# Performance work log

Measured on AMD Instinct MI355X. Metric: run time of the kernel, lower is better.

Reference implementation:

```python
import jax, jax.numpy as jnp
import numpy as np

B, N, D_IN, H, R = 4096, 32, 256, 256, 3
VIRTUAL_DECAY = 0.7


def setup_inputs() -> dict:
    key = jax.random.key(0)
    ks = jax.random.split(key, 16)
    def xavier(k, shape):
        fan_in, fan_out = shape[-1], shape[-2]
        lim = np.sqrt(6.0 / (fan_in + fan_out))
        return jax.random.uniform(k, shape, jnp.float32, -lim, lim)
    return {
        'input_vec': jax.random.normal(ks[0], (B, D_IN), jnp.float32),
        'child_h': jax.random.normal(ks[1], (B, N, H), jnp.float32),
        'child_c': jax.random.normal(ks[2], (B, N, H), jnp.float32),
        'relation_ids': jax.random.randint(ks[3], (B, N), 0, R, jnp.int32),
        'virtual_mask': jax.random.randint(ks[4], (B, N), 0, 2, jnp.int32).astype(bool),
        'rel_emb': xavier(ks[5], (R, H)),
        'W_i': xavier(ks[6], (H, D_IN + H)), 'b_i': jnp.full((H,), 0.1, jnp.float32),
        'W_f': xavier(ks[7], (R, H, H)),     'b_f': jnp.full((R, H), 0.1, jnp.float32),
        'W_o': xavier(ks[8], (H, D_IN + H)), 'b_o': jnp.full((H,), 0.1, jnp.float32),
        'W_u': xavier(ks[9], (H, D_IN + H)), 'b_u': jnp.full((H,), 0.1, jnp.float32),
        'w_att': xavier(ks[10], (1, H)).reshape(H), 'b_att': jnp.full((1,), 0.1, jnp.float32),
    }


def reference(input_vec, child_h, child_c, relation_ids, virtual_mask,
              rel_emb, W_i, b_i, W_f, b_f, W_o, b_o, W_u, b_u, w_att, b_att):
    # virtual-node decay applied to both child states
    decay = jnp.where(virtual_mask, VIRTUAL_DECAY, 1.0)[..., None]          # (B,N,1)
    ch = child_h * decay                                                     # (B,N,H)
    cc = child_c * decay                                                     # (B,N,H)

    # relation-aware attention over children (softmax over child axis)
    re = rel_emb[relation_ids]                                               # (B,N,H)
    scores = jnp.einsum('bnh,h->bn', re + ch, w_att) + b_att[0]              # (B,N)
    attn = jax.nn.softmax(scores, axis=1)[..., None]                         # (B,N,1)
    child_h_sum = jnp.sum(ch * attn, axis=1)                                 # (B,H)

    # relation-routed forget gates: compute all R linears, gather by relation id
    # NOTE: original applies NO sigmoid to f (faithful to source)
    f_all = jnp.einsum('bnh,rgh->bnrg', ch, W_f) + b_f                       # (B,N,R,H)
    f = jnp.take_along_axis(f_all, relation_ids[:, :, None, None], axis=2)[:, :, 0, :]  # (B,N,H)
    child_c_sum = jnp.sum(f * cc, axis=1)                                    # (B,H)

    combined = jnp.concatenate([input_vec, child_h_sum], axis=-1)            # (B,D_IN+H)
    i = jax.nn.sigmoid(combined @ W_i.T + b_i)
    o = jax.nn.sigmoid(combined @ W_o.T + b_o)
    u = jnp.tanh(combined @ W_u.T + b_u)
    c = i * u + child_c_sum
    h = o * jnp.tanh(c)
    return (h, c)
```

## Files before the change

### kernel.cpp

```cpp
#include <hip/hip_runtime.h>
#include <hip/hip_bf16.h>
#include <math.h>


#define B_    4096
#define N_    32
#define H_    256
#define DIN_  256
#define R_    3
#define MB    16
#define NBC   4
#define CHUNKS (MB / NBC)
#define DECAY 0.7f

#define WS_WF   0
#define WS_WI   196608
#define WS_WO   327680
#define WS_WU   458752
#define WS_ELEMS 589824

typedef __bf16 bf16;
typedef bf16  bf16x8 __attribute__((ext_vector_type(8)));
typedef float f32x4  __attribute__((ext_vector_type(4)));

__device__ __forceinline__ float sigmoidf_(float x) { return 1.0f / (1.0f + __expf(-x)); }

__device__ __forceinline__ bf16x8 cvt8_nt(const float* p) {
    f32x4 a = __builtin_nontemporal_load((const f32x4*)p);
    f32x4 b = __builtin_nontemporal_load((const f32x4*)(p + 4));
    bf16x8 r;
    #pragma unroll
    for (int j = 0; j < 4; ++j) { r[j] = (bf16)a[j]; r[j + 4] = (bf16)b[j]; }
    return r;
}
__device__ __forceinline__ bf16x8 cvt8_c(const float* p) {
    f32x4 a = *(const f32x4*)p;
    f32x4 b = *(const f32x4*)(p + 4);
    bf16x8 r;
    #pragma unroll
    for (int j = 0; j < 4; ++j) { r[j] = (bf16)a[j]; r[j + 4] = (bf16)b[j]; }
    return r;
}

template<bool WSW>
__device__ __forceinline__ bf16x8 ldw8(const bf16* wsp, const float* fp, int idx) {
    if constexpr (WSW) return *(const bf16x8*)(wsp + idx);
    else               return cvt8_c(fp + idx);
}

__global__ __launch_bounds__(256) void wprep(
    const float* __restrict__ Wf, const float* __restrict__ Wi,
    const float* __restrict__ Wo, const float* __restrict__ Wu,
    bf16* __restrict__ ws)
{
    int i = (blockIdx.x * 256 + threadIdx.x) * 8;
    const float* src; int off;
    if      (i < WS_WI) { src = Wf; off = i - WS_WF; }
    else if (i < WS_WO) { src = Wi; off = i - WS_WI; }
    else if (i < WS_WU) { src = Wo; off = i - WS_WO; }
    else                { src = Wu; off = i - WS_WU; }
    *(bf16x8*)(ws + i) = cvt8_c(src + off);
}

template<bool WSW>
__global__ __launch_bounds__(512) __attribute__((amdgpu_waves_per_eu(2, 2)))
void fused_main(
    const float* __restrict__ ivec,
    const float* __restrict__ child_h, const float* __restrict__ child_c,
    const int*  __restrict__ rel_ids,  const void* __restrict__ vmaskp,
    const float* __restrict__ rel_emb,
    const float* __restrict__ W_i, const float* __restrict__ b_i,
    const float* __restrict__ W_f, const float* __restrict__ b_f,
    const float* __restrict__ W_o, const float* __restrict__ b_o,
    const float* __restrict__ W_u, const float* __restrict__ b_u,
    const float* __restrict__ w_att, const float* __restrict__ b_att,
    const bf16* __restrict__ ws, float* __restrict__ out)
{
    __shared__ __align__(16) bf16 chs[NBC][N_][264];
    __shared__ __align__(16) bf16 hsumL[MB][264];
    __shared__ float csL[MB][H_];
    __shared__ float watt[H_];
    __shared__ float bfl[R_][H_];
    __shared__ float dall[MB][N_];
    __shared__ int   rids[MB][N_];
    __shared__ float scoreT[NBC * N_];
    __shared__ float rdotL[4];
    __shared__ int   m8flag;

    const int tid  = threadIdx.x;
    const int wave = tid >> 6;
    const int lane = tid & 63;
    const int t    = lane & 15;
    const int q    = lane >> 4;
    const int b0   = blockIdx.x * MB;

    const bf16* wfb = ws + WS_WF;
    const bf16* wib = ws + WS_WI;
    const bf16* wob = ws + WS_WO;
    const bf16* wub = ws + WS_WU;

    if (tid < 64) {
        const unsigned char* vb = (const unsigned char*)vmaskp;
        int bad = vb[tid * 4 + 1] | vb[tid * 4 + 2] | vb[tid * 4 + 3];
        unsigned long long any = __ballot(bad != 0);
        if (tid == 0) m8flag = (any != 0ull) ? 1 : 0;
    }
    __syncthreads();

    if (tid < H_) watt[tid] = w_att[tid];
    {
        int idx = b0 * N_ + tid;
        rids[tid >> 5][tid & 31] = rel_ids[idx];
        bool vm = m8flag ? (((const unsigned char*)vmaskp)[idx] != 0)
                         : (((const int*)vmaskp)[idx] != 0);
        dall[tid >> 5][tid & 31] = vm ? DECAY : 1.0f;
    }
    for (int i = tid; i < R_ * H_; i += 512) ((float*)bfl)[i] = b_f[i];
    if (tid == 0) rdotL[3] = b_att[0];
    __syncthreads();

    if (wave < R_) {
        int r = wave;
        float p = 0.f;
        #pragma unroll
        for (int j = 0; j < 4; ++j) {
            int h = lane * 4 + j;
            p += rel_emb[r * H_ + h] * watt[h];
        }
        #pragma unroll
        for (int off = 32; off >= 1; off >>= 1) p += __shfl_xor(p, off);
        if (lane == 0) rdotL[r] = p;
    }

    for (int ck = 0; ck < CHUNKS; ++ck) {
        __syncthreads();

        {
            size_t base = (size_t)(b0 + ck * NBC) * (N_ * H_);
            float dp[8];
            #pragma unroll
            for (int it = 0; it < 8; ++it) {
                int ge = (it * 512 + tid) << 3;
                int row = ge >> 8;
                int h = ge & 255;
                f32x4 a = __builtin_nontemporal_load((const f32x4*)(child_h + base + ge));
                f32x4 b = __builtin_nontemporal_load((const f32x4*)(child_h + base + ge + 4));
                bf16x8 r; float p = 0.f;
                #pragma unroll
                for (int j = 0; j < 4; ++j) {
                    r[j] = (bf16)a[j]; r[j + 4] = (bf16)b[j];
                    p += a[j] * watt[h + j] + b[j] * watt[h + 4 + j];
                }
                *(bf16x8*)(&chs[row >> 5][row & 31][h]) = r;
                dp[it] = p;
            }
            #pragma unroll
            for (int off = 16; off >= 1; off >>= 1) {
                #pragma unroll
                for (int it = 0; it < 8; ++it) dp[it] += __shfl_xor(dp[it], off);
            }
            if ((tid & 31) == 0) {
                int grp = tid >> 5;
                #pragma unroll
                for (int it = 0; it < 8; ++it) scoreT[it * 16 + grp] = dp[it];
            }
        }
        __syncthreads();

        float att0, att1;
        {
            int n  = lane & 31;
            int bi = lane >> 5;
            int bl0 = ck * NBC + bi, bl1 = bl0 + 2;
            float d0 = dall[bl0][n], d1 = dall[bl1][n];
            float s0 = d0 * scoreT[lane]      + rdotL[rids[bl0][n]] + rdotL[3];
            float s1 = d1 * scoreT[64 + lane] + rdotL[rids[bl1][n]] + rdotL[3];
            float m0 = s0, m1 = s1;
            #pragma unroll
            for (int off = 16; off >= 1; off >>= 1) {
                m0 = fmaxf(m0, __shfl_xor(m0, off));
                m1 = fmaxf(m1, __shfl_xor(m1, off));
            }
            float e0 = __expf(s0 - m0), e1 = __expf(s1 - m1);
            float u0 = e0, u1 = e1;
            #pragma unroll
            for (int off = 16; off >= 1; off >>= 1) {
                u0 += __shfl_xor(u0, off);
                u1 += __shfl_xor(u1, off);
            }
            att0 = (e0 / u0) * d0;
            att1 = (e1 / u1) * d1;
        }

        #pragma unroll
        for (int ps = 0; ps < 2; ++ps) {
            int bi = (tid >> 8) + ps * 2;
            int g  = tid & 255;
            int bl = ck * NBC + bi;
            float s = 0.f;
            #pragma unroll 8
            for (int n = 0; n < N_; ++n) {
                float av = __shfl(ps ? att1 : att0, ((tid >> 8) << 5) | n);
                s += av * (float)chs[bi][n][g];
            }
            hsumL[bl][g] = (bf16)s;
        }

        f32x4 acc[2][8];
        #pragma unroll
        for (int i = 0; i < 2; ++i)
            #pragma unroll
            for (int j = 0; j < 8; ++j)
                #pragma unroll
                for (int c = 0; c < 4; ++c) acc[i][j][c] = 0.0f;

        bf16x8 bzero;
        #pragma unroll
        for (int i = 0; i < 8; ++i) bzero[i] = (bf16)0.0f;

        int myrid[8];
        #pragma unroll
        for (int nt = 0; nt < 8; ++nt)
            myrid[nt] = rids[ck * NBC + (nt >> 1)][((nt & 1) << 4) + t];

        #pragma unroll
        for (int kc = 0; kc < 8; ++kc) {
            const int k = kc * 32 + q * 8;
            bf16x8 v[8];
            #pragma unroll
            for (int nt = 0; nt < 8; ++nt)
                v[nt] = *(const bf16x8*)(&chs[nt >> 1][((nt & 1) << 4) + t][k]);
            #pragma unroll
            for (int r = 0; r < R_; ++r) {
                bf16x8 afrag[2];
                #pragma unroll
                for (int m2 = 0; m2 < 2; ++m2) {
                    int g = (wave * 2 + m2) * 16 + t;
                    afrag[m2] = ldw8<WSW>(wfb, W_f, (r * H_ + g) * H_ + k);
                }
                #pragma unroll
                for (int nt = 0; nt < 8; ++nt) {
                    bf16x8 vm = (myrid[nt] == r) ? v[nt] : bzero;
                    acc[0][nt] = __builtin_amdgcn_mfma_f32_16x16x32_bf16(afrag[0], vm, acc[0][nt], 0, 0, 0);
                    acc[1][nt] = __builtin_amdgcn_mfma_f32_16x16x32_bf16(afrag[1], vm, acc[1][nt], 0, 0, 0);
                }
            }
        }

        {
            f32x4 cA[2][2], cB[2][2];
            {
                size_t cbase = (size_t)(b0 + ck * NBC) * (N_ * H_);
                #pragma unroll
                for (int m2 = 0; m2 < 2; ++m2)
                    #pragma unroll
                    for (int j = 0; j < 2; ++j)
                        cA[m2][j] = __builtin_nontemporal_load(
                            (const f32x4*)(child_c + cbase + (size_t)(((j << 4) + t)) * H_
                                           + (wave * 2 + m2) * 16 + q * 4));
            }
            #pragma unroll
            for (int bi = 0; bi < NBC; ++bi) {
                if (bi + 1 < NBC) {
                    size_t cbase = (size_t)(b0 + ck * NBC + bi + 1) * (N_ * H_);
                    #pragma unroll
                    for (int m2 = 0; m2 < 2; ++m2)
                        #pragma unroll
                        for (int j = 0; j < 2; ++j)
                            cB[m2][j] = __builtin_nontemporal_load(
                                (const f32x4*)(child_c + cbase + (size_t)(((j << 4) + t)) * H_
                                               + (wave * 2 + m2) * 16 + q * 4));
                }
                const int bl = ck * NBC + bi;
                #pragma unroll
                for (int m2 = 0; m2 < 2; ++m2) {
                    #pragma unroll
                    for (int reg = 0; reg < 4; ++reg) {
                        const int g = (wave * 2 + m2) * 16 + q * 4 + reg;
                        float p = 0.f;
                        #pragma unroll
                        for (int j = 0; j < 2; ++j) {
                            int nt = bi * 2 + j;
                            int n  = (j << 4) + t;
                            float d = dall[bl][n];
                            p += cA[m2][j][reg] * d
                                 * fmaf(d, acc[m2][nt][reg], bfl[rids[bl][n]][g]);
                        }
                        p += __shfl_xor(p, 1);
                        p += __shfl_xor(p, 2);
                        p += __shfl_xor(p, 4);
                        p += __shfl_xor(p, 8);
                        if (t == 0) csL[bl][g] = p;
                    }
                }
                if (bi + 1 < NBC) {
                    #pragma unroll
                    for (int m2 = 0; m2 < 2; ++m2)
                        #pragma unroll
                        for (int j = 0; j < 2; ++j)
                            cA[m2][j] = cB[m2][j];
                }
            }
        }
    }
    __syncthreads();

    const int j0 = wave * 32;
    f32x4 accI[2], accO[2], accU[2];
    #pragma unroll
    for (int c = 0; c < 2; ++c)
        #pragma unroll
        for (int r = 0; r < 4; ++r) { accI[c][r] = 0.f; accO[c][r] = 0.f; accU[c][r] = 0.f; }

    #pragma unroll
    for (int kc = 0; kc < 16; ++kc) {
        const int k = kc * 32 + q * 8;
        bf16x8 a;
        if (kc < 8) a = cvt8_nt(ivec + (size_t)(b0 + t) * DIN_ + k);
        else        a = *(const bf16x8*)(&hsumL[t][k - 256]);
        #pragma unroll
        for (int c = 0; c < 2; ++c) {
            int j = j0 + c * 16 + t;
            bf16x8 bI = ldw8<WSW>(wib, W_i, j * 512 + k);
            bf16x8 bO = ldw8<WSW>(wob, W_o, j * 512 + k);
            bf16x8 bU = ldw8<WSW>(wub, W_u, j * 512 + k);
            accI[c] = __builtin_amdgcn_mfma_f32_16x16x32_bf16(a, bI, accI[c], 0, 0, 0);
            accO[c] = __builtin_amdgcn_mfma_f32_16x16x32_bf16(a, bO, accO[c], 0, 0, 0);
            accU[c] = __builtin_amdgcn_mfma_f32_16x16x32_bf16(a, bU, accU[c], 0, 0, 0);
        }
    }

    #pragma unroll
    for (int c = 0; c < 2; ++c) {
        const int j = j0 + c * 16 + t;
        float biv = b_i[j], bov = b_o[j], buv = b_u[j];
        #pragma unroll
        for (int reg = 0; reg < 4; ++reg) {
            int bl = q * 4 + reg;
            size_t o1 = (size_t)(b0 + bl) * H_ + j;
            size_t o2 = (size_t)B_ * H_ + o1;
            float iv = sigmoidf_(accI[c][reg] + biv);
            float ov = sigmoidf_(accO[c][reg] + bov);
            float uv = tanhf(accU[c][reg] + buv);
            float cv = fmaf(iv, uv, csL[bl][j]);
            float hv = ov * tanhf(cv);
            __builtin_nontemporal_store(hv, out + o1);
            __builtin_nontemporal_store(cv, out + o2);
        }
    }
}

extern "C" void kernel_launch(void* const* d_in, const int* in_sizes, int n_in,
                              void* d_out, int out_size, void* d_ws, size_t ws_size,
                              hipStream_t stream)
{
    const float* ivec    = (const float*)d_in[0];
    const float* child_h = (const float*)d_in[1];
    const float* child_c = (const float*)d_in[2];
    const int*   relids  = (const int*)d_in[3];
    const void*  vmask   = d_in[4];
    const float* rel_emb = (const float*)d_in[5];
    const float* W_i     = (const float*)d_in[6];
    const float* b_i     = (const float*)d_in[7];
    const float* W_f     = (const float*)d_in[8];
    const float* b_f     = (const float*)d_in[9];
    const float* W_o     = (const float*)d_in[10];
    const float* b_o     = (const float*)d_in[11];
    const float* W_u     = (const float*)d_in[12];
    const float* b_u     = (const float*)d_in[13];
    const float* w_att   = (const float*)d_in[14];
    const float* b_att   = (const float*)d_in[15];
    float* out = (float*)d_out;
    bf16*  ws  = (bf16*)d_ws;

    const bool wsw = (ws_size >= (size_t)WS_ELEMS * sizeof(bf16));

    if (wsw) {
        hipLaunchKernelGGL(wprep, dim3(WS_ELEMS / 8 / 256), dim3(256), 0, stream,
                           W_f, W_i, W_o, W_u, ws);
        hipLaunchKernelGGL((fused_main<true>), dim3(B_ / MB), dim3(512), 0, stream,
                           ivec, child_h, child_c, relids, vmask, rel_emb,
                           W_i, b_i, W_f, b_f, W_o, b_o, W_u, b_u, w_att, b_att,
                           ws, out);
    } else {
        hipLaunchKernelGGL((fused_main<false>), dim3(B_ / MB), dim3(512), 0, stream,
                           ivec, child_h, child_c, relids, vmask, rel_emb,
                           W_i, b_i, W_f, b_f, W_o, b_o, W_u, b_u, w_att, b_att,
                           ws, out);
    }
}
```

Before: 420.8 us.

## Load child_h tiles directly into LDS as fp32 and spill child_c sums to output

Replaces the register-staged child_h load and bf16 conversion with global_load_lds async copies that place fp32 rows straight into shared memory. The attention dot products are then computed from LDS, and bf16 conversion moves into the MFMA operand fetch. The csL shared buffer is removed and the partial cell sum is written to the output buffer, then read back in the epilogue, which frees LDS for the larger fp32 tile. This doubles the LDS footprint of the child tile, adds conversion work inside the GEMM loop and adds a global round-trip for the cell sum.

```diff
diff --git a/kernel.cpp b/kernel.cpp
--- a/kernel.cpp
+++ b/kernel.cpp
@@ -12,6 +12,7 @@
 #define NBC   4
 #define CHUNKS (MB / NBC)
 #define DECAY 0.7f
+#define CHP   260
 
 #define WS_WF   0
 #define WS_WI   196608
@@ -22,6 +23,14 @@
 typedef __bf16 bf16;
 typedef bf16  bf16x8 __attribute__((ext_vector_type(8)));
 typedef float f32x4  __attribute__((ext_vector_type(4)));
+
+typedef unsigned int u32;
+typedef __attribute__((address_space(1))) const u32 gu32;
+typedef __attribute__((address_space(3))) u32 lu32;
+
+__device__ __forceinline__ void gll16(const void* g, void* l) {
+    __builtin_amdgcn_global_load_lds((gu32*)g, (lu32*)l, 16, 0, 0);
+}
 
 __device__ __forceinline__ float sigmoidf_(float x) { return 1.0f / (1.0f + __expf(-x)); }
 
@@ -76,9 +85,8 @@
     const float* __restrict__ w_att, const float* __restrict__ b_att,
     const bf16* __restrict__ ws, float* __restrict__ out)
 {
-    __shared__ __align__(16) bf16 chs[NBC][N_][264];
+    __shared__ __align__(16) float chsf[NBC][N_][CHP];
     __shared__ __align__(16) bf16 hsumL[MB][264];
-    __shared__ float csL[MB][H_];
     __shared__ float watt[H_];
     __shared__ float bfl[R_][H_];
     __shared__ float dall[MB][N_];
@@ -137,33 +145,29 @@
 
         {
             size_t base = (size_t)(b0 + ck * NBC) * (N_ * H_);
-            float dp[8];
-            #pragma unroll
-            for (int it = 0; it < 8; ++it) {
-                int ge = (it * 512 + tid) << 3;
-                int row = ge >> 8;
-                int h = ge & 255;
-                f32x4 a = __builtin_nontemporal_load((const f32x4*)(child_h + base + ge));
-                f32x4 b = __builtin_nontemporal_load((const f32x4*)(child_h + base + ge + 4));
-                bf16x8 r; float p = 0.f;
-                #pragma unroll
-                for (int j = 0; j < 4; ++j) {
-                    r[j] = (bf16)a[j]; r[j + 4] = (bf16)b[j];
-                    p += a[j] * watt[h + j] + b[j] * watt[h + 4 + j];
-                }
-                *(bf16x8*)(&chs[row >> 5][row & 31][h]) = r;
-                dp[it] = p;
-            }
-            #pragma unroll
-            for (int off = 16; off >= 1; off >>= 1) {
-                #pragma unroll
-                for (int it = 0; it < 8; ++it) dp[it] += __shfl_xor(dp[it], off);
-            }
-            if ((tid & 31) == 0) {
-                int grp = tid >> 5;
-                #pragma unroll
-                for (int it = 0; it < 8; ++it) scoreT[it * 16 + grp] = dp[it];
-            }
+            const float* src = child_h + base + lane * 4;
+            #pragma unroll
+            for (int i = 0; i < 16; ++i) {
+                int row = wave * 16 + i;
+                gll16(src + (size_t)row * H_, &chsf[row >> 5][row & 31][0]);
+            }
+        }
+        __syncthreads();
+
+        {
+            int row = tid >> 2, part = tid & 3;
+            const float* rp = &chsf[row >> 5][row & 31][part * 64];
+            const float* wp = &watt[part * 64];
+            float p = 0.f;
+            #pragma unroll
+            for (int jj = 0; jj < 16; ++jj) {
+                f32x4 v = *(const f32x4*)(rp + jj * 4);
+                #pragma unroll
+                for (int j = 0; j < 4; ++j) p += v[j] * wp[jj * 4 + j];
+            }
+            p += __shfl_xor(p, 1);
+            p += __shfl_xor(p, 2);
+            if (part == 0) scoreT[row] = p;
         }
         __syncthreads();
 
@@ -201,7 +205,7 @@
             #pragma unroll 8
             for (int n = 0; n < N_; ++n) {
                 float av = __shfl(ps ? att1 : att0, ((tid >> 8) << 5) | n);
-                s += av * (float)chs[bi][n][g];
+                s += av * chsf[bi][n][g];
             }
             hsumL[bl][g] = (bf16)s;
         }
@@ -228,8 +232,13 @@
             const int k = kc * 32 + q * 8;
             bf16x8 v[8];
             #pragma unroll
-            for (int nt = 0; nt < 8; ++nt)
-                v[nt] = *(const bf16x8*)(&chs[nt >> 1][((nt & 1) << 4) + t][k]);
+            for (int nt = 0; nt < 8; ++nt) {
+                const float* rp = &chsf[nt >> 1][((nt & 1) << 4) + t][k];
+                f32x4 va = *(const f32x4*)rp;
+                f32x4 vb = *(const f32x4*)(rp + 4);
+                #pragma unroll
+                for (int j = 0; j < 4; ++j) { v[nt][j] = (bf16)va[j]; v[nt][j + 4] = (bf16)vb[j]; }
+            }
             #pragma unroll
             for (int r = 0; r < R_; ++r) {
                 bf16x8 afrag[2];
@@ -290,7 +299,8 @@
                         p += __shfl_xor(p, 2);
                         p += __shfl_xor(p, 4);
                         p += __shfl_xor(p, 8);
-                        if (t == 0) csL[bl][g] = p;
+                        if (t == 0)
+                            out[(size_t)B_ * H_ + (size_t)(b0 + bl) * H_ + g] = p;
                     }
                 }
                 if (bi + 1 < NBC) {
@@ -339,10 +349,11 @@
             int bl = q * 4 + reg;
             size_t o1 = (size_t)(b0 + bl) * H_ + j;
             size_t o2 = (size_t)B_ * H_ + o1;
+            float csv = out[o2];
             float iv = sigmoidf_(accI[c][reg] + biv);
             float ov = sigmoidf_(accO[c][reg] + bov);
             float uv = tanhf(accU[c][reg] + buv);
-            float cv = fmaf(iv, uv, csL[bl][j]);
+            float cv = fmaf(iv, uv, csv);
             float hv = ov * tanhf(cv);
             __builtin_nontemporal_store(hv, out + o1);
             __builtin_nontemporal_store(cv, out + o2);
```

Measured after the change: 439.1 us. 1.04x slower.
